# Kernel tuning notes

Hardware: AMD Instinct MI355X
Metric: run time of the kernel (lower is better)

## Reference

```python
import jax, jax.numpy as jnp
import numpy as np

B, S, H = 4, 2048, 1024

def setup_inputs() -> dict:
    key = jax.random.key(0)
    ks = jax.random.split(key, 6)
    scale = 1.0 / np.sqrt(H)
    return {
        "query": jax.random.normal(ks[0], (B, S, H), dtype=jnp.float32),
        "key":   jax.random.normal(ks[1], (B, S, H), dtype=jnp.float32),
        "value": jax.random.normal(ks[2], (B, S, H), dtype=jnp.float32),
        "Wq": jax.random.normal(ks[3], (H, H), dtype=jnp.float32) * scale,
        "Wk": jax.random.normal(ks[4], (H, H), dtype=jnp.float32) * scale,
        "Wv": jax.random.normal(ks[5], (H, H), dtype=jnp.float32) * scale,
    }

def reference(query, key, value, Wq, Wk, Wv):
    # nn.Linear(bias=False): y = x @ W.T
    q = jnp.einsum('bsh,oh->bso', query, Wq)
    k = jnp.einsum('bsh,oh->bso', key, Wk)
    v = jnp.einsum('bsh,oh->bso', value, Wv)
    # full QK^T scores [B, Q, K], scaled by sqrt(hidden_size)
    scores = jnp.einsum('bqh,bkh->bqk', q, k) / jnp.sqrt(jnp.asarray(H, q.dtype))
    attn = jax.nn.softmax(scores, axis=2)
    return jnp.einsum('bqk,bkh->bqh', attn, v)
```

## Files before the change

kernel.cpp:

```cpp
#include <hip/hip_runtime.h>
#include <hip/hip_bf16.h>
#include <stdint.h>

#define BATCH 4
#define SLEN  2048
#define HID   1024

typedef __attribute__((ext_vector_type(8))) short bfrag8;
typedef __attribute__((ext_vector_type(4))) float facc4;
typedef __attribute__((ext_vector_type(4))) unsigned short us4;

__device__ __forceinline__ unsigned short f2b(float f) {
  union { float f; unsigned int i; } x; x.f = f;
  unsigned int r = x.i + 0x7FFFu + ((x.i >> 16) & 1u);
  return (unsigned short)(r >> 16);
}

__device__ __forceinline__ void gl_lds16(const void* g, void* l) {
  __builtin_amdgcn_global_load_lds(
      (const __attribute__((address_space(1))) void*)g,
      (__attribute__((address_space(3))) void*)l, 16, 0, 0);
}

__global__ __launch_bounds__(256) void cast_all(
    const float* __restrict__ q, const float* __restrict__ k,
    const float* __restrict__ v, const float* __restrict__ wq,
    const float* __restrict__ wk, const float* __restrict__ wv,
    us4* __restrict__ dst, float* __restrict__ lsum) {
  if (blockIdx.x < 8) {
    float4 z = {0.f, 0.f, 0.f, 0.f};
    ((float4*)lsum)[blockIdx.x * 256 + threadIdx.x] = z;
  }
  const long i = (long)blockIdx.x * 256 + threadIdx.x;
  const long S1 = 2097152, S2 = 4194304, S3 = 6291456,
             S4 = 6553600, S5 = 6815744;
  const float4* src; long off;
  if (i < S2) {
    if (i < S1) { src = (const float4*)q;  off = i; }
    else        { src = (const float4*)k;  off = i - S1; }
  } else if (i < S3) { src = (const float4*)v;  off = i - S2; }
  else if   (i < S4) { src = (const float4*)wq; off = i - S3; }
  else if   (i < S5) { src = (const float4*)wk; off = i - S4; }
  else               { src = (const float4*)wv; off = i - S5; }
  float4 x = src[off];
  us4 o;
  o.x = f2b(x.x); o.y = f2b(x.y); o.z = f2b(x.z); o.w = f2b(x.w);
  dst[i] = o;
}

__global__ __launch_bounds__(256) void proj3(
    const unsigned short* __restrict__ Xq, const unsigned short* __restrict__ Wqb,
    const unsigned short* __restrict__ Xk, const unsigned short* __restrict__ Wkb,
    const unsigned short* __restrict__ Xv, const unsigned short* __restrict__ Wvb,
    unsigned short* __restrict__ Qb, unsigned short* __restrict__ Kb,
    unsigned short* __restrict__ Vt) {
  const int pid = blockIdx.x;
  const int p2     = (pid & 7) * 192 + (pid >> 3);
  const int g      = p2 >> 9;
  const int within = p2 & 511;

  const unsigned short* A; const unsigned short* B; unsigned short* C;
  long bm, bn; int ldc_;
  if (g == 0)      { A = Xq; B = Wqb; C = Qb; }
  else if (g == 1) { A = Xk; B = Wkb; C = Kb; }
  else             { A = Wvb; B = Xv; C = Vt; }
  if (g < 2) {
    const int gid = within >> 5, rem = within & 31;
    bm = (long)(gid * 4 + (rem & 3)) * 128;
    bn = (long)(rem >> 2) * 128;
    ldc_ = 1024;
  } else {
    const int gid = within >> 8, rem = within & 255;
    bm = (long)(gid * 4 + (rem & 3)) * 128;
    bn = (long)(rem >> 2) * 128;
    ldc_ = 8192;
  }

  __shared__ __align__(16) unsigned short As[128 * 64];
  __shared__ __align__(16) unsigned short Bs[128 * 64];

  const int tid  = threadIdx.x;
  const int lane = tid & 63;
  const int wave = tid >> 6;
  const int wr   = (wave >> 1) * 64;
  const int wc   = (wave & 1) * 64;
  const int ln   = lane & 15;
  const int lq   = lane >> 4;
  const int swz  = ln & 7;

  facc4 acc[4][4] = {};

  const unsigned short* ap[4]; const unsigned short* bp[4];
  unsigned short* asd[4]; unsigned short* bsd[4];
#pragma unroll
  for (int j = 0; j < 4; ++j) {
    const int c   = j * 256 + tid;
    const int row = c >> 3;
    const int src = ((c & 7) ^ (row & 7)) * 8;
    ap[j]  = A + (bm + row) * 1024 + src;
    bp[j]  = B + (bn + row) * 1024 + src;
    asd[j] = &As[c * 8];
    bsd[j] = &Bs[c * 8];
  }

  for (int k0 = 0; k0 < 1024; k0 += 64) {
#pragma unroll
    for (int j = 0; j < 4; ++j) { gl_lds16(ap[j], asd[j]); ap[j] += 64; }
#pragma unroll
    for (int j = 0; j < 4; ++j) { gl_lds16(bp[j], bsd[j]); bp[j] += 64; }
    __syncthreads();

#pragma unroll
    for (int kk = 0; kk < 2; ++kk) {
      bfrag8 af[4], bfr[4];
#pragma unroll
      for (int i = 0; i < 4; ++i)
        af[i] = *(const bfrag8*)&As[(wr + i * 16 + ln) * 64 + ((kk * 4 + lq) ^ swz) * 8];
#pragma unroll
      for (int j = 0; j < 4; ++j)
        bfr[j] = *(const bfrag8*)&Bs[(wc + j * 16 + ln) * 64 + ((kk * 4 + lq) ^ swz) * 8];
#pragma unroll
      for (int i = 0; i < 4; ++i)
#pragma unroll
        for (int j = 0; j < 4; ++j)
          acc[i][j] = __builtin_amdgcn_mfma_f32_16x16x32_bf16(af[i], bfr[j], acc[i][j], 0, 0, 0);
    }
    __syncthreads();
  }

#pragma unroll
  for (int i = 0; i < 4; ++i)
#pragma unroll
    for (int j = 0; j < 4; ++j) {
      const long m = bm + wr + i * 16 + lq * 4;
      const long n = bn + wc + j * 16 + ln;
#pragma unroll
      for (int r = 0; r < 4; ++r)
        C[(m + r) * (long)ldc_ + n] = f2b(acc[i][j][r]);
    }
}

template <int MODE, typename OutT>
__global__ __launch_bounds__(256) void gemm_nt(
    const unsigned short* __restrict__ A, const unsigned short* __restrict__ B,
    OutT* __restrict__ C, int K, int lda, int ldb, int ldc,
    long aStrideZ, long bStrideZ, long cStrideZ, float alpha,
    float* __restrict__ lsum) {
  A += (long)blockIdx.z * aStrideZ;
  B += (long)blockIdx.z * bStrideZ;
  C += (long)blockIdx.z * cStrideZ;
  const long lz = (long)blockIdx.z * SLEN;

  const int nbm = gridDim.x, nbn = gridDim.y;
  const int nb  = nbm * nbn;
  const int pid = blockIdx.y * nbm + blockIdx.x;
  const int p2  = (pid & 7) * (nb >> 3) + (pid >> 3);
  const int GROUP = 4;
  const int gsize = GROUP * nbn;
  const int gid   = p2 / gsize;
  const int rem   = p2 - gid * gsize;
  const long bm = (long)(gid * GROUP + (rem & (GROUP - 1))) * 128;
  const long bn = (long)(rem >> 2) * 128;

  __shared__ __align__(16) unsigned short As[128 * 64];
  __shared__ __align__(16) unsigned short Bs[128 * 64];

  const int tid  = threadIdx.x;
  const int lane = tid & 63;
  const int wave = tid >> 6;
  const int wr   = (wave >> 1) * 64;
  const int wc   = (wave & 1) * 64;
  const int ln   = lane & 15;
  const int lq   = lane >> 4;
  const int swz  = ln & 7;

  facc4 acc[4][4] = {};

  const unsigned short* ap[4]; const unsigned short* bp[4];
  unsigned short* asd[4]; unsigned short* bsd[4];
#pragma unroll
  for (int j = 0; j < 4; ++j) {
    const int c   = j * 256 + tid;
    const int row = c >> 3;
    const int src = ((c & 7) ^ (row & 7)) * 8;
    ap[j]  = A + (bm + row) * (long)lda + src;
    bp[j]  = B + (bn + row) * (long)ldb + src;
    asd[j] = &As[c * 8];
    bsd[j] = &Bs[c * 8];
  }

  for (int k0 = 0; k0 < K; k0 += 64) {
#pragma unroll
    for (int j = 0; j < 4; ++j) { gl_lds16(ap[j], asd[j]); ap[j] += 64; }
#pragma unroll
    for (int j = 0; j < 4; ++j) { gl_lds16(bp[j], bsd[j]); bp[j] += 64; }
    __syncthreads();

#pragma unroll
    for (int kk = 0; kk < 2; ++kk) {
      bfrag8 af[4], bfr[4];
#pragma unroll
      for (int i = 0; i < 4; ++i)
        af[i] = *(const bfrag8*)&As[(wr + i * 16 + ln) * 64 + ((kk * 4 + lq) ^ swz) * 8];
#pragma unroll
      for (int j = 0; j < 4; ++j)
        bfr[j] = *(const bfrag8*)&Bs[(wc + j * 16 + ln) * 64 + ((kk * 4 + lq) ^ swz) * 8];
#pragma unroll
      for (int i = 0; i < 4; ++i)
#pragma unroll
        for (int j = 0; j < 4; ++j)
          acc[i][j] = __builtin_amdgcn_mfma_f32_16x16x32_bf16(af[i], bfr[j], acc[i][j], 0, 0, 0);
    }
    __syncthreads();
  }

  if constexpr (MODE == 1) {
#pragma unroll
    for (int i = 0; i < 4; ++i) {
#pragma unroll
      for (int r = 0; r < 4; ++r) {
        const long m = bm + wr + i * 16 + lq * 4 + r;
        float rowsum = 0.f;
#pragma unroll
        for (int j = 0; j < 4; ++j) {
          const long n = bn + wc + j * 16 + ln;
          float e = __expf(acc[i][j][r] * alpha);
          C[m * (long)ldc + n] = (OutT)f2b(e);
          rowsum += e;
        }
        rowsum += __shfl_xor(rowsum, 1, 64);
        rowsum += __shfl_xor(rowsum, 2, 64);
        rowsum += __shfl_xor(rowsum, 4, 64);
        rowsum += __shfl_xor(rowsum, 8, 64);
        if (ln == 0) atomicAdd(&lsum[lz + m], rowsum);
      }
    }
  } else {
    float inv[16];
#pragma unroll
    for (int i = 0; i < 4; ++i)
#pragma unroll
      for (int r = 0; r < 4; ++r)
        inv[i * 4 + r] = 1.0f / lsum[lz + bm + wr + i * 16 + lq * 4 + r];
#pragma unroll
    for (int i = 0; i < 4; ++i)
#pragma unroll
      for (int j = 0; j < 4; ++j) {
        const long m = bm + wr + i * 16 + lq * 4;
        const long n = bn + wc + j * 16 + ln;
#pragma unroll
        for (int r = 0; r < 4; ++r)
          ((float*)C)[(m + r) * (long)ldc + n] = acc[i][j][r] * inv[i * 4 + r];
      }
  }
}

extern "C" void kernel_launch(void* const* d_in, const int* in_sizes, int n_in,
                              void* d_out, int out_size, void* d_ws, size_t ws_size,
                              hipStream_t stream) {
  const float* q_in = (const float*)d_in[0];
  const float* k_in = (const float*)d_in[1];
  const float* v_in = (const float*)d_in[2];
  const float* wq   = (const float*)d_in[3];
  const float* wk   = (const float*)d_in[4];
  const float* wv   = (const float*)d_in[5];
  float* out = (float*)d_out;

  const long NXH = (long)BATCH * SLEN * HID;
  const long NW  = (long)HID * HID;
  const long SH  = (long)SLEN * HID;
  const long SS  = (long)SLEN * SLEN;

  unsigned short* ws = (unsigned short*)d_ws;
  unsigned short* Xq  = ws;
  unsigned short* Xk  = Xq  + NXH;
  unsigned short* Xv  = Xk  + NXH;
  unsigned short* Wqb = Xv  + NXH;
  unsigned short* Wkb = Wqb + NW;
  unsigned short* Wvb = Wkb + NW;
  unsigned short* Qb  = Wvb + NW;
  unsigned short* Kb  = Qb  + NXH;
  unsigned short* Vt  = Kb  + NXH;
  float*          lsum = (float*)(Vt + NXH);
  unsigned short* P   = Xq;

  const dim3 blk(256);

  cast_all<<<dim3(27648), blk, 0, stream>>>(q_in, k_in, v_in, wq, wk, wv,
                                            (us4*)ws, lsum);

  proj3<<<dim3(1536), blk, 0, stream>>>(Xq, Wqb, Xk, Wkb, Xv, Wvb, Qb, Kb, Vt);

  gemm_nt<1, unsigned short><<<dim3(16, 16, BATCH), blk, 0, stream>>>(
      Qb, Kb, P, HID, HID, HID, SLEN, SH, SH, SS, 0.03125f, lsum);

  gemm_nt<2, float><<<dim3(16, 8, BATCH), blk, 0, stream>>>(
      P, Vt, out, SLEN, SLEN, BATCH * SLEN, HID, SS, SLEN, SH, 1.0f, lsum);
}
```

Measured before the change: 298.0 us.

## Use 256x256 double-buffered MFMA core for projections and score GEMMs

Replaces the 128x128 single-buffered GEMM in the projection kernel and the scores GEMM with a 256x256-tile, 512-thread core. The core double-buffers LDS through global_load_lds, interleaves the next tile's loads with MFMA phases, and raises wave priority around the MFMAs. This is meant to increase operand reuse per LDS load and overlap memory with compute. In exchange it needs 128KB of dynamic shared memory, which limits occupancy to one block per CU. The grid is also small (256 blocks for scores), which may under-fill the CUs.

Result: no change. 294.0 us (-1.3%).

```diff
diff --git a/kernel.cpp b/kernel.cpp
--- a/kernel.cpp
+++ b/kernel.cpp
@@ -48,96 +48,197 @@
   dst[i] = o;
 }
 
-__global__ __launch_bounds__(256) void proj3(
+__device__ __forceinline__ void core256(
+    const unsigned short* __restrict__ A, const unsigned short* __restrict__ B,
+    const int lda, const int ldb, const int NT,
+    unsigned short* __restrict__ As, unsigned short* __restrict__ Bs,
+    facc4 (&acc)[8][4]) {
+  const int tid  = threadIdx.x;
+  const int lane = tid & 63;
+  const int wave = tid >> 6;
+  const int wm = wave >> 2;
+  const int wn = wave & 3;
+  const int ln = lane & 15;
+  const int lq = lane >> 4;
+  const int swz = ln & 7;
+
+  const int row0 = tid >> 3;
+  const int blk  = (tid & 7) ^ (row0 & 7);
+  const unsigned short* pA = A + (long)row0 * lda + blk * 8;
+  const unsigned short* pB = B + (long)row0 * ldb + blk * 8;
+  const long a64 = 64l * lda, b64 = 64l * ldb;
+  unsigned short* dA = As + tid * 8;
+  unsigned short* dB = Bs + tid * 8;
+
+#define STG_A(h, b, t) do { const unsigned short* g_ = pA + (h) * (a64 * 2) + (long)(t) * 64; \
+    gl_lds16(g_,       dA + (b) * 16384 + (h) * 8192); \
+    gl_lds16(g_ + a64, dA + (b) * 16384 + (h) * 8192 + 4096); } while (0)
+#define STG_B(h, b, t) do { const unsigned short* g_ = pB + (h) * (b64 * 2) + (long)(t) * 64; \
+    gl_lds16(g_,       dB + (b) * 16384 + (h) * 8192); \
+    gl_lds16(g_ + b64, dB + (b) * 16384 + (h) * 8192 + 4096); } while (0)
+
+  const int o0 = (lq ^ swz) * 8;
+  const int o1 = ((4 + lq) ^ swz) * 8;
+  const int aOfs = wm * 8192 + ln * 64;
+  const int bOfs = (wn >> 1) * 8192 + ((wn & 1) * 64 + ln) * 64;
+
+  STG_A(0, 0, 0); STG_A(1, 0, 0); STG_B(0, 0, 0); STG_B(1, 0, 0);
+  STG_A(0, 1, 1); STG_A(1, 1, 1);
+  asm volatile("s_waitcnt vmcnt(4)" ::: "memory");
+  __builtin_amdgcn_s_barrier();
+
+#define MFMA16(AF, BF, MOFS, NOFS)                                          \
+  _Pragma("unroll") for (int m_ = 0; m_ < 4; ++m_)                          \
+  _Pragma("unroll") for (int n_ = 0; n_ < 2; ++n_) {                        \
+    acc[(MOFS) + m_][(NOFS) + n_] = __builtin_amdgcn_mfma_f32_16x16x32_bf16(\
+        AF[m_][0], BF[n_][0], acc[(MOFS) + m_][(NOFS) + n_], 0, 0, 0);      \
+    acc[(MOFS) + m_][(NOFS) + n_] = __builtin_amdgcn_mfma_f32_16x16x32_bf16(\
+        AF[m_][1], BF[n_][1], acc[(MOFS) + m_][(NOFS) + n_], 0, 0, 0);      \
+  }
+
+  for (int t = 0; t < NT; ++t) {
+    const int bu = t & 1, nx = bu ^ 1;
+    const unsigned short* Ab = As + bu * 16384 + aOfs;
+    const unsigned short* Bb = Bs + bu * 16384 + bOfs;
+    bfrag8 a0[4][2], a1[4][2], b0[2][2], b1[2][2];
+
+#pragma unroll
+    for (int m = 0; m < 4; ++m) {
+      a0[m][0] = *(const bfrag8*)(Ab + m * 1024 + o0);
+      a0[m][1] = *(const bfrag8*)(Ab + m * 1024 + o1);
+    }
+#pragma unroll
+    for (int n = 0; n < 2; ++n) {
+      b0[n][0] = *(const bfrag8*)(Bb + n * 1024 + o0);
+      b0[n][1] = *(const bfrag8*)(Bb + n * 1024 + o1);
+    }
+    if (t + 1 < NT) STG_B(0, nx, t + 1);
+    __builtin_amdgcn_s_barrier();
+    __builtin_amdgcn_s_setprio(1);
+    MFMA16(a0, b0, 0, 0)
+    __builtin_amdgcn_s_setprio(0);
+    __builtin_amdgcn_s_barrier();
+
+#pragma unroll
+    for (int m = 0; m < 4; ++m) {
+      a1[m][0] = *(const bfrag8*)(Ab + (4 + m) * 1024 + o0);
+      a1[m][1] = *(const bfrag8*)(Ab + (4 + m) * 1024 + o1);
+    }
+#pragma unroll
+    for (int n = 0; n < 2; ++n) {
+      b1[n][0] = *(const bfrag8*)(Bb + (2 + n) * 1024 + o0);
+      b1[n][1] = *(const bfrag8*)(Bb + (2 + n) * 1024 + o1);
+    }
+    if (t + 1 < NT) STG_B(1, nx, t + 1);
+    __builtin_amdgcn_s_barrier();
+    __builtin_amdgcn_s_setprio(1);
+    MFMA16(a1, b1, 4, 2)
+    __builtin_amdgcn_s_setprio(0);
+    __builtin_amdgcn_s_barrier();
+
+    if (t + 2 < NT) STG_A(0, bu, t + 2);
+    __builtin_amdgcn_s_setprio(1);
+    MFMA16(a0, b1, 0, 2)
+    __builtin_amdgcn_s_setprio(0);
+    __builtin_amdgcn_s_barrier();
+
+    if (t + 2 < NT) STG_A(1, bu, t + 2);
+    __builtin_amdgcn_s_setprio(1);
+    MFMA16(a1, b0, 4, 0)
+    __builtin_amdgcn_s_setprio(0);
+    if (t + 2 < NT) asm volatile("s_waitcnt vmcnt(4)" ::: "memory");
+    else            asm volatile("s_waitcnt vmcnt(0)" ::: "memory");
+    __builtin_amdgcn_s_barrier();
+  }
+#undef MFMA16
+#undef STG_A
+#undef STG_B
+}
+
+__global__ __launch_bounds__(512, 2) void proj3_256(
     const unsigned short* __restrict__ Xq, const unsigned short* __restrict__ Wqb,
     const unsigned short* __restrict__ Xk, const unsigned short* __restrict__ Wkb,
     const unsigned short* __restrict__ Xv, const unsigned short* __restrict__ Wvb,
     unsigned short* __restrict__ Qb, unsigned short* __restrict__ Kb,
     unsigned short* __restrict__ Vt) {
+  extern __shared__ unsigned short smem[];
+  unsigned short* As = smem;
+  unsigned short* Bs = smem + 32768;
+
   const int pid = blockIdx.x;
-  const int p2     = (pid & 7) * 192 + (pid >> 3);
-  const int g      = p2 >> 9;
-  const int within = p2 & 511;
+  const int p2  = (pid & 7) * 48 + (pid >> 3);
+  const int g   = p2 >> 7;
+  const int within = p2 & 127;
 
   const unsigned short* A; const unsigned short* B; unsigned short* C;
   long bm, bn; int ldc_;
-  if (g == 0)      { A = Xq; B = Wqb; C = Qb; }
-  else if (g == 1) { A = Xk; B = Wkb; C = Kb; }
-  else             { A = Wvb; B = Xv; C = Vt; }
-  if (g < 2) {
-    const int gid = within >> 5, rem = within & 31;
-    bm = (long)(gid * 4 + (rem & 3)) * 128;
-    bn = (long)(rem >> 2) * 128;
-    ldc_ = 1024;
-  } else {
-    const int gid = within >> 8, rem = within & 255;
-    bm = (long)(gid * 4 + (rem & 3)) * 128;
-    bn = (long)(rem >> 2) * 128;
-    ldc_ = 8192;
-  }
-
-  __shared__ __align__(16) unsigned short As[128 * 64];
-  __shared__ __align__(16) unsigned short Bs[128 * 64];
-
-  const int tid  = threadIdx.x;
-  const int lane = tid & 63;
-  const int wave = tid >> 6;
-  const int wr   = (wave >> 1) * 64;
-  const int wc   = (wave & 1) * 64;
-  const int ln   = lane & 15;
-  const int lq   = lane >> 4;
-  const int swz  = ln & 7;
-
-  facc4 acc[4][4] = {};
-
-  const unsigned short* ap[4]; const unsigned short* bp[4];
-  unsigned short* asd[4]; unsigned short* bsd[4];
-#pragma unroll
-  for (int j = 0; j < 4; ++j) {
-    const int c   = j * 256 + tid;
-    const int row = c >> 3;
-    const int src = ((c & 7) ^ (row & 7)) * 8;
-    ap[j]  = A + (bm + row) * 1024 + src;
-    bp[j]  = B + (bn + row) * 1024 + src;
-    asd[j] = &As[c * 8];
-    bsd[j] = &Bs[c * 8];
-  }
-
-  for (int k0 = 0; k0 < 1024; k0 += 64) {
-#pragma unroll
-    for (int j = 0; j < 4; ++j) { gl_lds16(ap[j], asd[j]); ap[j] += 64; }
-#pragma unroll
-    for (int j = 0; j < 4; ++j) { gl_lds16(bp[j], bsd[j]); bp[j] += 64; }
-    __syncthreads();
-
-#pragma unroll
-    for (int kk = 0; kk < 2; ++kk) {
-      bfrag8 af[4], bfr[4];
-#pragma unroll
-      for (int i = 0; i < 4; ++i)
-        af[i] = *(const bfrag8*)&As[(wr + i * 16 + ln) * 64 + ((kk * 4 + lq) ^ swz) * 8];
-#pragma unroll
-      for (int j = 0; j < 4; ++j)
-        bfr[j] = *(const bfrag8*)&Bs[(wc + j * 16 + ln) * 64 + ((kk * 4 + lq) ^ swz) * 8];
-#pragma unroll
-      for (int i = 0; i < 4; ++i)
-#pragma unroll
-        for (int j = 0; j < 4; ++j)
-          acc[i][j] = __builtin_amdgcn_mfma_f32_16x16x32_bf16(af[i], bfr[j], acc[i][j], 0, 0, 0);
-    }
-    __syncthreads();
-  }
-
-#pragma unroll
-  for (int i = 0; i < 4; ++i)
-#pragma unroll
-    for (int j = 0; j < 4; ++j) {
-      const long m = bm + wr + i * 16 + lq * 4;
-      const long n = bn + wc + j * 16 + ln;
+  if (g == 0)      { A = Xq;  B = Wqb; C = Qb; }
+  else if (g == 1) { A = Xk;  B = Wkb; C = Kb; }
+  else             { A = Wvb; B = Xv;  C = Vt; }
+  if (g < 2) { bm = (long)(within >> 2) * 256; bn = (long)(within & 3)  * 256; ldc_ = 1024; }
+  else       { bm = (long)(within >> 5) * 256; bn = (long)(within & 31) * 256; ldc_ = 8192; }
+
+  facc4 acc[8][4] = {};
+  core256(A + bm * 1024, B + bn * 1024, 1024, 1024, HID / 64, As, Bs, acc);
+
+  const int lane = threadIdx.x & 63, wave = threadIdx.x >> 6;
+  const int wm = wave >> 2, wn = wave & 3;
+  const int ln = lane & 15, lq = lane >> 4;
+#pragma unroll
+  for (int m = 0; m < 8; ++m)
+#pragma unroll
+    for (int n = 0; n < 4; ++n) {
+      const long mm = bm + wm * 128 + m * 16 + lq * 4;
+      const long nn = bn + wn * 64 + n * 16 + ln;
 #pragma unroll
       for (int r = 0; r < 4; ++r)
-        C[(m + r) * (long)ldc_ + n] = f2b(acc[i][j][r]);
-    }
+        C[(mm + r) * (long)ldc_ + nn] = f2b(acc[m][n][r]);
+    }
+}
+
+__global__ __launch_bounds__(512, 2) void scores256(
+    const unsigned short* __restrict__ Q, const unsigned short* __restrict__ Kb,
+    unsigned short* __restrict__ P, float* __restrict__ lsum) {
+  extern __shared__ unsigned short smem[];
+  unsigned short* As = smem;
+  unsigned short* Bs = smem + 32768;
+
+  const long z = blockIdx.z;
+  const int pid = blockIdx.y * 8 + blockIdx.x;
+  const int p2  = (pid & 7) * 8 + (pid >> 3);
+  const long bm = (long)(p2 >> 3) * 256;
+  const long bn = (long)(p2 & 7) * 256;
+
+  const long SH = (long)SLEN * HID, SS = (long)SLEN * SLEN;
+  facc4 acc[8][4] = {};
+  core256(Q + z * SH + bm * 1024, Kb + z * SH + bn * 1024, 1024, 1024,
+          HID / 64, As, Bs, acc);
+
+  unsigned short* Pz = P + z * SS;
+  float* lz = lsum + z * SLEN;
+  const int lane = threadIdx.x & 63, wave = threadIdx.x >> 6;
+  const int wm = wave >> 2, wn = wave & 3;
+  const int ln = lane & 15, lq = lane >> 4;
+#pragma unroll
+  for (int m = 0; m < 8; ++m) {
+#pragma unroll
+    for (int r = 0; r < 4; ++r) {
+      const long q = bm + wm * 128 + m * 16 + lq * 4 + r;
+      float rowsum = 0.f;
+#pragma unroll
+      for (int n = 0; n < 4; ++n) {
+        const long kcol = bn + wn * 64 + n * 16 + ln;
+        float e = __expf(acc[m][n][r] * 0.03125f);
+        Pz[q * (long)SLEN + kcol] = f2b(e);
+        rowsum += e;
+      }
+      rowsum += __shfl_xor(rowsum, 1, 64);
+      rowsum += __shfl_xor(rowsum, 2, 64);
+      rowsum += __shfl_xor(rowsum, 4, 64);
+      rowsum += __shfl_xor(rowsum, 8, 64);
+      if (ln == 0) atomicAdd(&lz[q], rowsum);
+    }
+  }
 }
 
 template <int MODE, typename OutT>
@@ -284,16 +385,23 @@
   float*          lsum = (float*)(Vt + NXH);
   unsigned short* P   = Xq;
 
-  const dim3 blk(256);
-
-  cast_all<<<dim3(27648), blk, 0, stream>>>(q_in, k_in, v_in, wq, wk, wv,
-                                            (us4*)ws, lsum);
-
-  proj3<<<dim3(1536), blk, 0, stream>>>(Xq, Wqb, Xk, Wkb, Xv, Wvb, Qb, Kb, Vt);
-
-  gemm_nt<1, unsigned short><<<dim3(16, 16, BATCH), blk, 0, stream>>>(
-      Qb, Kb, P, HID, HID, HID, SLEN, SH, SH, SS, 0.03125f, lsum);
-
-  gemm_nt<2, float><<<dim3(16, 8, BATCH), blk, 0, stream>>>(
+  static bool attr_done = false;
+  if (!attr_done) {
+    hipFuncSetAttribute(reinterpret_cast<const void*>(proj3_256),
+                        hipFuncAttributeMaxDynamicSharedMemorySize, 131072);
+    hipFuncSetAttribute(reinterpret_cast<const void*>(scores256),
+                        hipFuncAttributeMaxDynamicSharedMemorySize, 131072);
+    attr_done = true;
+  }
+
+  cast_all<<<dim3(27648), dim3(256), 0, stream>>>(q_in, k_in, v_in, wq, wk, wv,
+                                                  (us4*)ws, lsum);
+
+  proj3_256<<<dim3(384), dim3(512), 131072, stream>>>(
+      Xq, Wqb, Xk, Wkb, Xv, Wvb, Qb, Kb, Vt);
+
+  scores256<<<dim3(8, 8, BATCH), dim3(512), 131072, stream>>>(Qb, Kb, P, lsum);
+
+  gemm_nt<2, float><<<dim3(16, 8, BATCH), dim3(256), 0, stream>>>(
       P, Vt, out, SLEN, SLEN, BATCH * SLEN, HID, SS, SLEN, SH, 1.0f, lsum);
 }
```
